# Kernel optimization log

Hardware: AMD Instinct MI355X
Metric: run time of the kernel (lower is better)

The kernel has to match this reference:

```python
import jax, jax.numpy as jnp
import numpy as np

IMG = 640.0  # pixel coordinate range for keypoints


def setup_inputs() -> dict:
    key = jax.random.key(0)
    ks = jax.random.split(key, 16)
    B, N, M, C, D, G = 4, 4096, 4096, 256, 256, 32
    s = 1.0 / np.sqrt(C)
    inp = {
        "nodes_t": jax.random.normal(ks[0], (B, N, C), jnp.float32),
        "nodes_t1": jax.random.normal(ks[1], (B, M, C), jnp.float32),
        "kpts_t1_pred": jax.random.uniform(ks[2], (B, N, 2), jnp.float32) * IMG,
        "kpts_t1_actual": jax.random.uniform(ks[3], (B, M, 2), jnp.float32) * IMG,
        "Wq": jax.random.normal(ks[4], (D, C), jnp.float32) * s,
        "bq": jnp.zeros((D,), jnp.float32),
        "Wk": jax.random.normal(ks[5], (D, C), jnp.float32) * s,
        "bk": jnp.zeros((D,), jnp.float32),
        "Wv": jax.random.normal(ks[6], (D, C), jnp.float32) * s,
        "bv": jnp.zeros((D,), jnp.float32),
        "Wm": jax.random.normal(ks[7], (D, D), jnp.float32) * (1.0 / np.sqrt(D)),
        "bm": jnp.zeros((D,), jnp.float32),
        "Wg1": jax.random.normal(ks[8], (G, 3), jnp.float32) * (1.0 / np.sqrt(3.0)),
        "bg1": jnp.zeros((G,), jnp.float32),
        "Wg2": jax.random.normal(ks[9], (G, G), jnp.float32) * (1.0 / np.sqrt(G)),
        "bg2": jnp.zeros((G,), jnp.float32),
        "iter_idx": 0,
    }
    return inp


def reference(nodes_t, nodes_t1, kpts_t1_pred, kpts_t1_actual,
              Wq, bq, Wk, bk, Wv, bv, Wm, bm, Wg1, bg1, Wg2, bg2, iter_idx):
    # window size schedule (iter_idx is a static Python int)
    win = 64.0 if iter_idx == 0 else max(4.0, 32.0 / 2 ** (iter_idx - 1))

    Q = nodes_t @ Wq.T + bq      # [B,N,256]
    K = nodes_t1 @ Wk.T + bk     # [B,M,256]
    V = nodes_t1 @ Wv.T + bv     # [B,M,256]

    # distance-based window mask [B,N,M]
    du = jnp.abs(kpts_t1_pred[:, :, 0:1] - kpts_t1_actual[:, None, :, 0])
    dv = jnp.abs(kpts_t1_pred[:, :, 1:2] - kpts_t1_actual[:, None, :, 1])
    mask = (du < win) & (dv < win)

    attn = jnp.einsum('bnd,bmd->bnm', Q, K) / jnp.sqrt(jnp.float32(256.0))
    attn = jnp.where(mask, attn, jnp.float32(-1e9))
    w = jax.nn.softmax(attn, axis=-1)

    matched_features = jnp.einsum('bnm,bmd->bnd', w, V)        # [B,N,256]
    matched_kpts = jnp.einsum('bnm,bmc->bnc', w, kpts_t1_actual)  # [B,N,2]

    confidence = jnp.any(mask, axis=-1, keepdims=True).astype(jnp.float32)  # [B,N,1]
    flow_residual = (matched_kpts - kpts_t1_pred) * confidence

    geo_in = jnp.concatenate([flow_residual, confidence], axis=-1)  # [B,N,3]
    h = jax.nn.silu(geo_in @ Wg1.T + bg1)
    geo_temp = h @ Wg2.T + bg2                                   # [B,N,32]

    merged = matched_features @ Wm.T + bm                        # [B,N,256]
    return merged, geo_temp, flow_residual, confidence
```

## Files before the change

### kernel.cpp

```cpp
#include <hip/hip_runtime.h>
#include <hip/hip_bf16.h>

typedef unsigned short ushort;
typedef unsigned int uint;
typedef __bf16 bf16x8 __attribute__((ext_vector_type(8)));
typedef float f32x4 __attribute__((ext_vector_type(4)));
typedef ushort ushort8 __attribute__((ext_vector_type(8)));

#define LOG2E 1.4426950408889634f
#define MFMA16(a,b,c) __builtin_amdgcn_mfma_f32_16x16x32_bf16((a),(b),(c),0,0,0)
#define GLL16(src, dst) __builtin_amdgcn_global_load_lds( \
    (const __attribute__((address_space(1))) void*)(src), \
    (__attribute__((address_space(3))) void*)(dst), 16, 0, 0)
#define GLL4(src, dst) __builtin_amdgcn_global_load_lds( \
    (const __attribute__((address_space(1))) void*)(src), \
    (__attribute__((address_space(3))) void*)(dst), 4, 0, 0)

static __device__ __forceinline__ uint packbf(float lo, float hi) {
  union { __bf16 h[2]; uint u; } x;
  x.h[0] = (__bf16)lo; x.h[1] = (__bf16)hi;
  return x.u;
}
static __device__ __forceinline__ int cellof(float x) {
  int c = (int)(x * 0.015625f);
  return c < 0 ? 0 : (c > 9 ? 9 : c);
}

__global__ __launch_bounds__(256) void cast_weights(
    const float* __restrict__ W0, const float* __restrict__ W1,
    const float* __restrict__ W2, const float* __restrict__ W3,
    __bf16* __restrict__ out,
    int* __restrict__ hist, int* __restrict__ curs, float* __restrict__ meanN)
{
  if (blockIdx.x == 0 && blockIdx.y == 0) {
    int t = threadIdx.x;
    for (int i = t; i < 1024; i += 256) { hist[i] = 0; curs[i] = 0; meanN[i] = 0.f; }
  }
  const int which = blockIdx.y;
  const float* src = which == 0 ? W0 : which == 1 ? W1 : which == 2 ? W2 : W3;
  const int i = (blockIdx.x * 256 + threadIdx.x) * 4;
  f32x4 v = *(const f32x4*)(src + i);
  union { __bf16 h[4]; uint u[2]; } x;
  #pragma unroll
  for (int j = 0; j < 4; j++) x.h[j] = (__bf16)v[j];
  *(uint*)(out + (size_t)which * 65536 + i) = x.u[0];
  *(uint*)(out + (size_t)which * 65536 + i + 2) = x.u[1];
}

__global__ __launch_bounds__(256) void cast_nodes(
    const float* __restrict__ n0, const float* __restrict__ n1,
    __bf16* __restrict__ o0, __bf16* __restrict__ o1)
{
  const float* s = blockIdx.y ? n1 : n0;
  __bf16* o = blockIdx.y ? o1 : o0;
  const int i = (blockIdx.x * 256 + threadIdx.x) * 4;
  f32x4 v = *(const f32x4*)(s + i);
  union { __bf16 h[4]; uint u[2]; } x;
  #pragma unroll
  for (int j = 0; j < 4; j++) x.h[j] = (__bf16)v[j];
  *(uint*)(o + i) = x.u[0];
  *(uint*)(o + i + 2) = x.u[1];
}

__global__ __launch_bounds__(256) void hist_kernel(
    const float* __restrict__ kpred, const float* __restrict__ kact,
    int* __restrict__ hist, int* __restrict__ cellpt)
{
  int p = blockIdx.x * 256 + threadIdx.x;
  int type = p >> 14, idx = p & 16383;
  const float2 c = ((const float2*)(type == 0 ? kpred : kact))[idx];
  int cell = cellof(c.x) * 10 + cellof(c.y);
  int b = idx >> 12;
  atomicAdd(&hist[(type * 4 + b) * 128 + cell], 1);
  cellpt[type * 16384 + idx] = cell;
}

__global__ __launch_bounds__(256) void scan_kernel(
    const int* __restrict__ hist, int* __restrict__ strt, int* __restrict__ curs)
{
  __shared__ int sh[1024];
  int t = threadIdx.x;
  for (int i = t; i < 1024; i += 256) sh[i] = hist[i];
  __syncthreads();
  if (t < 8) {
    int run = 0;
    for (int c = 0; c < 100; c++) {
      strt[t * 128 + c] = run;
      curs[t * 128 + c] = run;
      run += sh[t * 128 + c];
    }
    strt[t * 128 + 100] = run;
  }
}

__global__ __launch_bounds__(256) void scatter_kernel(
    const float* __restrict__ kpred, const float* __restrict__ kact,
    const int* __restrict__ cellpt, int* __restrict__ curs,
    int* __restrict__ sq, int* __restrict__ invq, float* __restrict__ kpS,
    int* __restrict__ sk, int* __restrict__ invk, float* __restrict__ kaS)
{
  int p = blockIdx.x * 256 + threadIdx.x;
  int type = p >> 14, idx = p & 16383;
  int b = idx >> 12, n = idx & 4095;
  int cell = cellpt[type * 16384 + idx];
  int pos = atomicAdd(&curs[(type * 4 + b) * 128 + cell], 1);
  if (type == 0) {
    sq[b * 4096 + pos] = n;
    invq[b * 4096 + n] = pos;
    ((float2*)kpS)[b * 4096 + pos] = ((const float2*)kpred)[idx];
  } else {
    sk[b * 4096 + pos] = n;
    invk[b * 4096 + n] = pos;
    ((float2*)kaS)[b * 4096 + pos] = ((const float2*)kact)[idx];
  }
}

__global__ __launch_bounds__(256) void meansum_kernel(
    const float* __restrict__ nodes_t1, float* __restrict__ meanN)
{
  int b = blockIdx.y, chunk = blockIdx.x, c = threadIdx.x;
  const float* base = nodes_t1 + ((size_t)b * 4096 + chunk * 256) * 256 + c;
  float s = 0.f;
  for (int r = 0; r < 256; r++) s += base[(size_t)r * 256];
  atomicAdd(&meanN[b * 256 + c], s);
}

__global__ __launch_bounds__(256) void vmean_kernel(
    const float* __restrict__ meanN, const float* __restrict__ Wv,
    const float* __restrict__ bv, float* __restrict__ Vmean)
{
  __shared__ float mn[256];
  int b = blockIdx.x, d = threadIdx.x;
  mn[d] = meanN[b * 256 + d] * (1.0f / 4096.0f);
  __syncthreads();
  float s = bv[d];
  const float* w = Wv + (size_t)d * 256;
  for (int c = 0; c < 256; c++) s += mn[c] * w[c];
  Vmean[b * 256 + d] = s;
}

__global__ __launch_bounds__(256) void gemm_qkv(
    const ushort* __restrict__ A0, const ushort* __restrict__ A1,
    const ushort* __restrict__ W4,
    const float* __restrict__ bq, const float* __restrict__ bk,
    const float* __restrict__ bv,
    __bf16* __restrict__ outQ, __bf16* __restrict__ outK,
    __bf16* __restrict__ outVs,
    const int* __restrict__ invq, const int* __restrict__ invk)
{
  const int z = blockIdx.z;
  const ushort* A = z == 0 ? A0 : A1;
  const ushort* Wa = z == 0 ? W4 : W4 + 65536;
  const ushort* Wb = W4 + 131072;
  const int* inv = z == 0 ? invq : invk;

  const int wid = threadIdx.x >> 6;
  const int lane = threadIdx.x & 63;
  const int q = lane & 15, g = lane >> 4;
  const int nb = blockIdx.x * 64 + (wid >> 1) * 32;
  const int db = blockIdx.y * 128 + (wid & 1) * 64;

  f32x4 acc[2][4], accv[2][4];
  #pragma unroll
  for (int a = 0; a < 2; a++)
    #pragma unroll
    for (int b = 0; b < 4; b++) {
      acc[a][b] = f32x4{0.f,0.f,0.f,0.f};
      accv[a][b] = f32x4{0.f,0.f,0.f,0.f};
    }

  const ushort* Wa0 = Wa + (size_t)(db + q) * 256 + g * 8;
  const ushort* Wb0 = Wb + (size_t)(db + q) * 256 + g * 8;
  const ushort* Ar0 = A + (size_t)(nb + q) * 256 + g * 8;
  const ushort* Ar1 = A + (size_t)(nb + 16 + q) * 256 + g * 8;

  #pragma unroll
  for (int c0 = 0; c0 < 256; c0 += 32) {
    bf16x8 a0 = *(const bf16x8*)(Ar0 + c0);
    bf16x8 a1 = *(const bf16x8*)(Ar1 + c0);
    #pragma unroll
    for (int df = 0; df < 4; df++) {
      bf16x8 w = *(const bf16x8*)(Wa0 + df * 16 * 256 + c0);
      acc[0][df] = MFMA16(a0, w, acc[0][df]);
      acc[1][df] = MFMA16(a1, w, acc[1][df]);
    }
    if (z == 1) {
      #pragma unroll
      for (int df = 0; df < 4; df++) {
        bf16x8 w = *(const bf16x8*)(Wb0 + df * 16 * 256 + c0);
        accv[0][df] = MFMA16(a0, w, accv[0][df]);
        accv[1][df] = MFMA16(a1, w, accv[1][df]);
      }
    }
  }
  const float* biasA = z == 0 ? bq : bk;
  __bf16* oA = z == 0 ? outQ : outK;
  #pragma unroll
  for (int df = 0; df < 4; df++) {
    float ba = biasA[db + df * 16 + q];
    float bb = bv[db + df * 16 + q];
    #pragma unroll
    for (int nf = 0; nf < 2; nf++)
      #pragma unroll
      for (int r = 0; r < 4; r++) {
        int row = nb + nf * 16 + g * 4 + r;
        int d = db + df * 16 + q;
        int pos = inv[row];
        size_t orow = (size_t)(row & ~4095) + pos;
        oA[orow * 256 + d] = (__bf16)(acc[nf][df][r] + ba);
        if (z == 1)
          outVs[orow * 256 + d] = (__bf16)(accv[nf][df][r] + bb);
      }
  }
}

__global__ __launch_bounds__(256) void transpose_v(
    const ushort* __restrict__ Vs, ushort* __restrict__ VT)
{
  __shared__ ushort tile[64][76];
  const int b = blockIdx.z, rt = blockIdx.x, dt = blockIdx.y;
  const int tid = threadIdx.x;
  const ushort* src = Vs + ((size_t)b * 4096 + rt * 64) * 256 + dt * 64;
  #pragma unroll
  for (int i = 0; i < 2; i++) {
    int c = tid + i * 256;
    int r = c >> 3, dc = (c & 7) * 8;
    ushort8 v = *(const ushort8*)(src + (size_t)r * 256 + dc);
    #pragma unroll
    for (int j = 0; j < 8; j++) tile[r][dc + j] = v[j];
  }
  __syncthreads();
  ushort* dst = VT + ((size_t)b * 256 + dt * 64) * 4096 + rt * 64;
  #pragma unroll
  for (int i = 0; i < 2; i++) {
    int c = tid + i * 256;
    int d = c >> 3, rc = (c & 7) * 8;
    ushort8 v;
    #pragma unroll
    for (int j = 0; j < 8; j++) v[j] = tile[rc + j][d];
    *(ushort8*)(dst + (size_t)d * 4096 + rc) = v;
  }
}

__global__ __launch_bounds__(256) void gemm_merged(
    const ushort* __restrict__ A, const ushort* __restrict__ W,
    const float* __restrict__ bias, float* __restrict__ out)
{
  const int wid = threadIdx.x >> 6;
  const int lane = threadIdx.x & 63;
  const int q = lane & 15, g = lane >> 4;
  const int nb = blockIdx.x * 64 + (wid >> 1) * 32;
  const int db = blockIdx.y * 128 + (wid & 1) * 64;

  f32x4 acc[2][4];
  #pragma unroll
  for (int a = 0; a < 2; a++)
    #pragma unroll
    for (int b = 0; b < 4; b++) acc[a][b] = f32x4{0.f,0.f,0.f,0.f};

  const ushort* W0 = W + (size_t)(db + q) * 256 + g * 8;
  const ushort* Ar0 = A + (size_t)(nb + q) * 256 + g * 8;
  const ushort* Ar1 = A + (size_t)(nb + 16 + q) * 256 + g * 8;

  #pragma unroll
  for (int c0 = 0; c0 < 256; c0 += 32) {
    bf16x8 a0 = *(const bf16x8*)(Ar0 + c0);
    bf16x8 a1 = *(const bf16x8*)(Ar1 + c0);
    #pragma unroll
    for (int df = 0; df < 4; df++) {
      bf16x8 w = *(const bf16x8*)(W0 + df * 16 * 256 + c0);
      acc[0][df] = MFMA16(a0, w, acc[0][df]);
      acc[1][df] = MFMA16(a1, w, acc[1][df]);
    }
  }
  #pragma unroll
  for (int df = 0; df < 4; df++) {
    float bval = bias[db + df * 16 + q];
    #pragma unroll
    for (int nf = 0; nf < 2; nf++)
      #pragma unroll
      for (int r = 0; r < 4; r++) {
        int row = nb + nf * 16 + g * 4 + r;
        out[(size_t)row * 256 + db + df * 16 + q] = acc[nf][df][r] + bval;
      }
  }
}

__global__ __launch_bounds__(256, 2) void attn_kernel(
    const ushort* __restrict__ Q,
    const ushort* __restrict__ K,
    const ushort* __restrict__ VT,
    const float* __restrict__ kpS,
    const int* __restrict__ iter_idx,
    const int* __restrict__ sq,
    const int* __restrict__ strt,
    const float* __restrict__ kaS,
    const float* __restrict__ Vmean,
    __bf16* __restrict__ matched,
    float* __restrict__ out_flow, float* __restrict__ out_conf)
{
  __shared__ __align__(16) ushort Kl[2][8192];
  __shared__ __align__(16) ushort Vl[2][8192];
  __shared__ __align__(16) float2 Cl[2][32];
  __shared__ int tl_t[132], tl_ks[132], tl_ke[132];
  __shared__ int ntile_s;

  const int tid = threadIdx.x;
  const int wid = tid >> 6, lane = tid & 63;
  const int q = lane & 15, g = lane >> 4;
  const int orig = blockIdx.x;
  const int wgid = (orig & 7) * 50 + (orig >> 3);
  const int batch = wgid / 100;
  const int cell = wgid % 100;

  const int qstart = strt[batch * 128 + cell];
  const int nq = strt[batch * 128 + cell + 1] - qstart;
  if (nq == 0) return;

  const int cu = cell / 10, cv = cell % 10;
  const int c0 = cv > 0 ? cv - 1 : 0, c1 = cv < 9 ? cv + 1 : 9;
  const int* kst = strt + (4 + batch) * 128;

  if (tid == 0) {
    int n = 0;
    int lo = cu > 0 ? cu - 1 : 0, hi = cu < 9 ? cu + 1 : 9;
    for (int cc = lo; cc <= hi; cc++) {
      int ks = kst[cc * 10 + c0];
      int ke = kst[cc * 10 + c1 + 1];
      for (int t = ks & ~31; t < ke; t += 32) {
        tl_t[n] = t; tl_ks[n] = ks; tl_ke[n] = ke; n++;
      }
    }
    ntile_s = n;
  }
  __syncthreads();
  const int ntile = ntile_s;

  const int idx = *iter_idx;
  const float win = (idx == 0) ? 64.0f : fmaxf(4.0f, ldexpf(32.0f, 1 - idx));

  const ushort* Kbase = K + (size_t)batch * 4096 * 256;
  const ushort* VTb = VT + (size_t)batch * 1048576;
  const float* kasf = kaS + (size_t)batch * 8192;
  const float* Vm = Vmean + batch * 256;

  const int npass = (nq + 63) >> 6;

  auto STAGE = [&](int ti, int b) {
    const int t = tl_t[ti];
    #pragma unroll
    for (int j = 0; j < 4; j++) {
      int n = wid * 256 + j * 64 + lane;
      int r = n & 31, u = n >> 5;
      GLL16(Kbase + (size_t)(t + r) * 256 + u * 8,
            &Kl[b][(size_t)(wid * 256 + j * 64) * 8]);
    }
    #pragma unroll
    for (int j = 0; j < 4; j++) {
      int n = wid * 256 + j * 64 + lane;
      int pl = n >> 8, d = n & 255;
      GLL16(VTb + (size_t)d * 4096 + t + pl * 8,
            &Vl[b][(size_t)(wid * 256 + j * 64) * 8]);
    }
    if (wid == 0) GLL4(kasf + t * 2 + lane, &Cl[b][0]);
  };

  int cnt = 0, qi = 0;
  bool active = false;
  float pu = 0.f, pv = 0.f;
  bf16x8 qf[8];
  f32x4 O[16];
  float m_run = -1e9f, l_run = 0.f, u_run = 0.f, v_run = 0.f;

  auto PASS_INIT = [&](int pp) {
    int tbase = pp * 64 + wid * 16;
    active = tbase < nq;
    cnt = active ? min(16, nq - tbase) : 0;
    if (active) {
      int qq = q < cnt ? q : cnt - 1;
      int qsrow = batch * 4096 + qstart + tbase + qq;
      qi = sq[qsrow];
      const ushort* qptr = Q + (size_t)qsrow * 256 + g * 8;
      #pragma unroll
      for (int mf = 0; mf < 8; mf++) qf[mf] = *(const bf16x8*)(qptr + mf * 32);
      float2 kpv = ((const float2*)kpS)[qsrow];
      pu = kpv.x; pv = kpv.y;
    }
    #pragma unroll
    for (int i = 0; i < 16; i++) O[i] = f32x4{0.f,0.f,0.f,0.f};
    m_run = -1e9f; l_run = 0.f; u_run = 0.f; v_run = 0.f;
  };

  auto EPILOGUE = [&]() {
    if (!active) return;
    l_run += __shfl_xor(l_run, 16); l_run += __shfl_xor(l_run, 32);
    u_run += __shfl_xor(u_run, 16); u_run += __shfl_xor(u_run, 32);
    v_run += __shfl_xor(v_run, 16); v_run += __shfl_xor(v_run, 32);
    bool degen = (m_run <= -5e8f) || (l_run == 0.f);
    float rinv = degen ? 0.f : 1.0f / l_run;
    if (g == 0 && q < cnt) {
      float conf = degen ? 0.f : 1.0f;
      int row = batch * 4096 + qi;
      float fu = (u_run * rinv - pu) * conf, fv = (v_run * rinv - pv) * conf;
      ((float2*)out_flow)[row] = float2{fu, fv};
      out_conf[row] = conf;
    }
    #pragma unroll
    for (int r = 0; r < 4; r++) {
      int src = 4 * g + r;
      int qi_r = __shfl(qi, src);
      float il_r = __shfl(rinv, src);
      bool dg_r = (il_r == 0.f);
      if (src < cnt) {
        __bf16* mrow = matched + ((size_t)batch * 4096 + qi_r) * 256;
        #pragma unroll
        for (int df = 0; df < 16; df++) {
          float val = dg_r ? Vm[df * 16 + q] : O[df][r] * il_r;
          mrow[df * 16 + q] = (__bf16)val;
        }
      }
    }
  };

  if (ntile == 0) {
    for (int pp = 0; pp < npass; pp++) { PASS_INIT(pp); EPILOGUE(); }
    return;
  }

  const int total = npass * ntile;
  STAGE(0, 0);
  PASS_INIT(0);

  int i = 0, pp = 0;
  for (int it = 0; it < total; ++it) {
    __syncthreads();
    if (it + 1 < total) {
      int ni = (i + 1 == ntile) ? 0 : i + 1;
      STAGE(ni, (it + 1) & 1);
    }
    const int b = it & 1;

    if (active) {
      const int t = tl_t[i], ks = tl_ks[i], ke = tl_ke[i];

      f32x4 s0a = {0.f,0.f,0.f,0.f}, s0b = {0.f,0.f,0.f,0.f};
      f32x4 s1a = {0.f,0.f,0.f,0.f}, s1b = {0.f,0.f,0.f,0.f};
      #pragma unroll
      for (int mf = 0; mf < 8; mf += 2) {
        bf16x8 ka0 = *(const bf16x8*)&Kl[b][(size_t)(((mf    ) * 4 + g) * 32 + q     ) * 8];
        bf16x8 kb0 = *(const bf16x8*)&Kl[b][(size_t)(((mf + 1) * 4 + g) * 32 + q     ) * 8];
        bf16x8 ka1 = *(const bf16x8*)&Kl[b][(size_t)(((mf    ) * 4 + g) * 32 + q + 16) * 8];
        bf16x8 kb1 = *(const bf16x8*)&Kl[b][(size_t)(((mf + 1) * 4 + g) * 32 + q + 16) * 8];
        s0a = MFMA16(ka0, qf[mf],     s0a);
        s0b = MFMA16(kb0, qf[mf + 1], s0b);
        s1a = MFMA16(ka1, qf[mf],     s1a);
        s1b = MFMA16(kb1, qf[mf + 1], s1b);
      }

      float aus[8], avs[8], sv[8];
      #pragma unroll
      for (int r = 0; r < 4; r++) {
        int jr = t + 4 * g + r;
        float2 cc0 = Cl[b][4 * g + r];
        aus[r] = cc0.x; avs[r] = cc0.y;
        bool val = (jr >= ks && jr < ke);
        float du = fabsf(pu - cc0.x), dv = fabsf(pv - cc0.y);
        float sr = s0a[r] + s0b[r];
        sv[r] = (val && fmaxf(du, dv) < win) ? sr * 0.0625f : -1e9f;

        int jr1 = jr + 16;
        float2 cc1 = Cl[b][16 + 4 * g + r];
        aus[4 + r] = cc1.x; avs[4 + r] = cc1.y;
        val = (jr1 >= ks && jr1 < ke);
        du = fabsf(pu - cc1.x); dv = fabsf(pv - cc1.y);
        sr = s1a[r] + s1b[r];
        sv[4 + r] = (val && fmaxf(du, dv) < win) ? sr * 0.0625f : -1e9f;
      }

      float mt = fmaxf(fmaxf(fmaxf(sv[0], sv[1]), fmaxf(sv[2], sv[3])),
                       fmaxf(fmaxf(sv[4], sv[5]), fmaxf(sv[6], sv[7])));
      mt = fmaxf(mt, __shfl_xor(mt, 16));
      mt = fmaxf(mt, __shfl_xor(mt, 32));
      if (__any(mt > m_run + 8.0f)) {
        float m_new = fmaxf(m_run, mt);
        float scale = exp2f((m_run - m_new) * LOG2E);
        l_run *= scale; u_run *= scale; v_run *= scale;
        float s_r[4];
        #pragma unroll
        for (int r = 0; r < 4; r++) s_r[r] = __shfl(scale, 4 * g + r);
        #pragma unroll
        for (int df = 0; df < 16; df++)
          #pragma unroll
          for (int r = 0; r < 4; r++) O[df][r] *= s_r[r];
        m_run = m_new;
      }

      float p[8];
      #pragma unroll
      for (int ii = 0; ii < 8; ii++) p[ii] = exp2f((sv[ii] - m_run) * LOG2E);
      #pragma unroll
      for (int ii = 0; ii < 8; ii++) {
        l_run += p[ii];
        u_run += p[ii] * aus[ii];
        v_run += p[ii] * avs[ii];
      }

      uint d0 = packbf(p[0], p[1]), d1 = packbf(p[2], p[3]);
      uint d2 = packbf(p[4], p[5]), d3 = packbf(p[6], p[7]);
      int srcA = q + ((g & 1) << 5);
      int srcB = srcA + 16;
      uint x0 = (uint)__shfl((int)d0, srcA), x1 = (uint)__shfl((int)d1, srcA);
      uint x2 = (uint)__shfl((int)d0, srcB), x3 = (uint)__shfl((int)d1, srcB);
      uint y0 = (uint)__shfl((int)d2, srcA), y1 = (uint)__shfl((int)d3, srcA);
      uint y2 = (uint)__shfl((int)d2, srcB), y3 = (uint)__shfl((int)d3, srcB);
      union { uint i4[4]; bf16x8 v; } af;
      bool lo = (g < 2);
      af.i4[0] = lo ? x0 : y0; af.i4[1] = lo ? x1 : y1;
      af.i4[2] = lo ? x2 : y2; af.i4[3] = lo ? x3 : y3;

      #pragma unroll
      for (int df = 0; df < 16; df++) {
        bf16x8 vfd = *(const bf16x8*)&Vl[b][(size_t)(g * 256 + df * 16 + q) * 8];
        O[df] = MFMA16(af.v, vfd, O[df]);
      }
    }

    if (i == ntile - 1) {
      EPILOGUE();
      pp++;
      if (pp < npass) PASS_INIT(pp);
      i = 0;
    } else {
      i++;
    }
  }
}

__global__ __launch_bounds__(256) void geo_kernel(
    const float* __restrict__ flow, const float* __restrict__ conf_in,
    const float* __restrict__ Wg1, const float* __restrict__ bg1,
    const float* __restrict__ Wg2, const float* __restrict__ bg2,
    float* __restrict__ out_geo)
{
  __shared__ float w1[32][3], b1[32], b2[32];
  __shared__ __align__(16) float w2[32][32];
  int tid = threadIdx.x;
  for (int i = tid; i < 96; i += 256) w1[i / 3][i % 3] = Wg1[i];
  if (tid < 32) { b1[tid] = bg1[tid]; b2[tid] = bg2[tid]; }
  for (int i = tid; i < 1024; i += 256) w2[i / 32][i % 32] = Wg2[i];
  __syncthreads();

  int row = blockIdx.x * 256 + tid;
  float2 f = ((const float2*)flow)[row];
  float c = conf_in[row];
  float h[32];
  #pragma unroll
  for (int j = 0; j < 32; j++) {
    float x = w1[j][0] * f.x + w1[j][1] * f.y + w1[j][2] * c + b1[j];
    h[j] = x / (1.f + __expf(-x));
  }
  #pragma unroll
  for (int o = 0; o < 32; o += 2) {
    float s0 = b2[o], s1 = b2[o + 1];
    #pragma unroll
    for (int j = 0; j < 32; j += 4) {
      f32x4 wa = *(const f32x4*)&w2[o][j];
      f32x4 wb = *(const f32x4*)&w2[o + 1][j];
      s0 += wa[0]*h[j] + wa[1]*h[j+1] + wa[2]*h[j+2] + wa[3]*h[j+3];
      s1 += wb[0]*h[j] + wb[1]*h[j+1] + wb[2]*h[j+2] + wb[3]*h[j+3];
    }
    ((float2*)out_geo)[((size_t)row * 32 + o) >> 1] = float2{s0, s1};
  }
}

extern "C" void kernel_launch(void* const* d_in, const int* in_sizes, int n_in,
                              void* d_out, int out_size, void* d_ws, size_t ws_size,
                              hipStream_t stream) {
  const float* nodes_t  = (const float*)d_in[0];
  const float* nodes_t1 = (const float*)d_in[1];
  const float* kpred    = (const float*)d_in[2];
  const float* kact     = (const float*)d_in[3];
  const float* Wq = (const float*)d_in[4];  const float* bq = (const float*)d_in[5];
  const float* Wk = (const float*)d_in[6];  const float* bk = (const float*)d_in[7];
  const float* Wv = (const float*)d_in[8];  const float* bv = (const float*)d_in[9];
  const float* Wm = (const float*)d_in[10]; const float* bm = (const float*)d_in[11];
  const float* Wg1= (const float*)d_in[12]; const float* bg1= (const float*)d_in[13];
  const float* Wg2= (const float*)d_in[14]; const float* bg2= (const float*)d_in[15];
  const int* iter = (const int*)d_in[16];

  float* out_merged = (float*)d_out;
  float* out_geo  = out_merged + 4 * 4096 * 32 * 8;
  out_geo = out_merged + 4 * 4096 * 256;
  float* out_flow = out_geo + 4 * 4096 * 32;
  float* out_conf = out_flow + 4 * 4096 * 2;

  ushort* wsQ   = (ushort*)d_ws;
  ushort* wsK   = wsQ + 4194304;
  ushort* wsVT  = wsK + 4194304;
  ushort* wsM   = wsVT + 4194304;
  ushort* wsW   = wsM + 4194304;
  float*  kaS   = (float*)(wsW + 262144);
  float*  kpS   = kaS + 32768;
  float*  meanN = kpS + 32768;
  float*  Vmean = meanN + 1024;
  int*    hist  = (int*)(Vmean + 1024);
  int*    strt  = hist + 1024;
  int*    curs  = strt + 1024;
  int*    cellpt= curs + 1024;
  int*    sq    = cellpt + 32768;
  int*    sk    = sq + 16384;
  int*    invk  = sk + 16384;
  int*    invq  = invk + 16384;
  ushort* wsA0  = (ushort*)(invq + 16384);
  ushort* wsA1  = wsA0 + 4194304;

  dim3 cg(64, 4, 1);
  cast_weights<<<cg, 256, 0, stream>>>(Wq, Wk, Wv, Wm, (__bf16*)wsW,
                                       hist, curs, meanN);
  dim3 ng(4096, 2, 1);
  cast_nodes<<<ng, 256, 0, stream>>>(nodes_t, nodes_t1,
                                     (__bf16*)wsA0, (__bf16*)wsA1);
  hist_kernel<<<128, 256, 0, stream>>>(kpred, kact, hist, cellpt);
  scan_kernel<<<1, 256, 0, stream>>>(hist, strt, curs);
  scatter_kernel<<<128, 256, 0, stream>>>(kpred, kact, cellpt, curs,
                                          sq, invq, kpS, sk, invk, kaS);
  dim3 mg(16, 4, 1);
  meansum_kernel<<<mg, 256, 0, stream>>>(nodes_t1, meanN);
  vmean_kernel<<<4, 256, 0, stream>>>(meanN, Wv, bv, Vmean);

  dim3 qg(256, 2, 2);
  gemm_qkv<<<qg, 256, 0, stream>>>(wsA0, wsA1, wsW, bq, bk, bv,
                                   (__bf16*)wsQ, (__bf16*)wsK, (__bf16*)wsM,
                                   invq, invk);
  dim3 tg(64, 4, 4);
  transpose_v<<<tg, 256, 0, stream>>>(wsM, wsVT);
  attn_kernel<<<400, 256, 0, stream>>>(wsQ, wsK, wsVT, kpS, iter,
                                       sq, strt, kaS, Vmean,
                                       (__bf16*)wsM, out_flow, out_conf);
  dim3 gg(256, 2, 1);
  gemm_merged<<<gg, 256, 0, stream>>>(wsM, wsW + 196608, bm, out_merged);
  geo_kernel<<<64, 256, 0, stream>>>(out_flow, out_conf, Wg1, bg1, Wg2, bg2, out_geo);
}
```

Baseline: 205.8 us.

## Fuse prep kernels, merge gemm with geo, and XOR-swizzle K/V LDS tiles

Several small setup kernels (weight cast, node cast, histogram, mean-sum) are merged into one launch, with a memset replacing the in-kernel zeroing. Scan and V-mean are merged, and the output GEMM is merged with the geo MLP into one launch. Separately, the attention kernel's K and V shared-memory tiles get an XOR swizzle to reduce LDS bank conflicts on fragment reads. The aim is less launch overhead and fewer conflicts, in exchange for heavier branching inside the fused kernels.

```diff
diff --git a/kernel.cpp b/kernel.cpp
--- a/kernel.cpp
+++ b/kernel.cpp
@@ -26,70 +26,87 @@
   return c < 0 ? 0 : (c > 9 ? 9 : c);
 }
 
-__global__ __launch_bounds__(256) void cast_weights(
-    const float* __restrict__ W0, const float* __restrict__ W1,
-    const float* __restrict__ W2, const float* __restrict__ W3,
-    __bf16* __restrict__ out,
-    int* __restrict__ hist, int* __restrict__ curs, float* __restrict__ meanN)
+__global__ __launch_bounds__(256) void prep_kernel(
+    const float* __restrict__ Wq, const float* __restrict__ Wk,
+    const float* __restrict__ Wv, const float* __restrict__ Wm,
+    __bf16* __restrict__ wsW,
+    const float* __restrict__ n0, const float* __restrict__ n1,
+    __bf16* __restrict__ a0, __bf16* __restrict__ a1,
+    const float* __restrict__ kpred, const float* __restrict__ kact,
+    int* __restrict__ hist, int* __restrict__ cellpt,
+    float* __restrict__ meanN)
 {
-  if (blockIdx.x == 0 && blockIdx.y == 0) {
-    int t = threadIdx.x;
-    for (int i = t; i < 1024; i += 256) { hist[i] = 0; curs[i] = 0; meanN[i] = 0.f; }
-  }
-  const int which = blockIdx.y;
-  const float* src = which == 0 ? W0 : which == 1 ? W1 : which == 2 ? W2 : W3;
-  const int i = (blockIdx.x * 256 + threadIdx.x) * 4;
-  f32x4 v = *(const f32x4*)(src + i);
-  union { __bf16 h[4]; uint u[2]; } x;
-  #pragma unroll
-  for (int j = 0; j < 4; j++) x.h[j] = (__bf16)v[j];
-  *(uint*)(out + (size_t)which * 65536 + i) = x.u[0];
-  *(uint*)(out + (size_t)which * 65536 + i + 2) = x.u[1];
-}
-
-__global__ __launch_bounds__(256) void cast_nodes(
-    const float* __restrict__ n0, const float* __restrict__ n1,
-    __bf16* __restrict__ o0, __bf16* __restrict__ o1)
-{
-  const float* s = blockIdx.y ? n1 : n0;
-  __bf16* o = blockIdx.y ? o1 : o0;
-  const int i = (blockIdx.x * 256 + threadIdx.x) * 4;
-  f32x4 v = *(const f32x4*)(s + i);
-  union { __bf16 h[4]; uint u[2]; } x;
-  #pragma unroll
-  for (int j = 0; j < 4; j++) x.h[j] = (__bf16)v[j];
-  *(uint*)(o + i) = x.u[0];
-  *(uint*)(o + i + 2) = x.u[1];
-}
-
-__global__ __launch_bounds__(256) void hist_kernel(
-    const float* __restrict__ kpred, const float* __restrict__ kact,
-    int* __restrict__ hist, int* __restrict__ cellpt)
-{
-  int p = blockIdx.x * 256 + threadIdx.x;
-  int type = p >> 14, idx = p & 16383;
-  const float2 c = ((const float2*)(type == 0 ? kpred : kact))[idx];
-  int cell = cellof(c.x) * 10 + cellof(c.y);
-  int b = idx >> 12;
-  atomicAdd(&hist[(type * 4 + b) * 128 + cell], 1);
-  cellpt[type * 16384 + idx] = cell;
-}
-
-__global__ __launch_bounds__(256) void scan_kernel(
-    const int* __restrict__ hist, int* __restrict__ strt, int* __restrict__ curs)
+  const int bid = blockIdx.x, tid = threadIdx.x;
+  if (bid < 64) {
+    const int which = bid >> 4;
+    const float* src = which == 0 ? Wq : which == 1 ? Wk : which == 2 ? Wv : Wm;
+    const int i = (bid & 15) * 4096 + tid * 16;
+    #pragma unroll
+    for (int j2 = 0; j2 < 4; j2++) {
+      f32x4 v = *(const f32x4*)(src + i + j2 * 4);
+      union { __bf16 h[4]; uint u[2]; } x;
+      #pragma unroll
+      for (int j = 0; j < 4; j++) x.h[j] = (__bf16)v[j];
+      *(uint*)(wsW + (size_t)which * 65536 + i + j2 * 4) = x.u[0];
+      *(uint*)(wsW + (size_t)which * 65536 + i + j2 * 4 + 2) = x.u[1];
+    }
+  } else if (bid < 8256) {
+    const int k = bid - 64;
+    const float* s = k < 4096 ? n0 : n1;
+    __bf16* o = k < 4096 ? a0 : a1;
+    const int i = (k & 4095) * 1024 + tid * 4;
+    f32x4 v = *(const f32x4*)(s + i);
+    union { __bf16 h[4]; uint u[2]; } x;
+    #pragma unroll
+    for (int j = 0; j < 4; j++) x.h[j] = (__bf16)v[j];
+    *(uint*)(o + i) = x.u[0];
+    *(uint*)(o + i + 2) = x.u[1];
+  } else if (bid < 8384) {
+    const int p = (bid - 8256) * 256 + tid;
+    const int type = p >> 14, idx = p & 16383;
+    const float2 c = ((const float2*)(type == 0 ? kpred : kact))[idx];
+    const int cell = cellof(c.x) * 10 + cellof(c.y);
+    const int b = idx >> 12;
+    atomicAdd(&hist[(type * 4 + b) * 128 + cell], 1);
+    cellpt[type * 16384 + idx] = cell;
+  } else {
+    const int mb = bid - 8384;
+    const int b = mb >> 4, chunk = mb & 15;
+    const float* base = n1 + ((size_t)b * 4096 + chunk * 256) * 256 + tid;
+    float s = 0.f;
+    for (int r = 0; r < 256; r++) s += base[(size_t)r * 256];
+    atomicAdd(&meanN[b * 256 + tid], s);
+  }
+}
+
+__global__ __launch_bounds__(256) void scan_vmean(
+    const int* __restrict__ hist, int* __restrict__ strt, int* __restrict__ curs,
+    const float* __restrict__ meanN, const float* __restrict__ Wv,
+    const float* __restrict__ bv, float* __restrict__ Vmean)
 {
   __shared__ int sh[1024];
-  int t = threadIdx.x;
-  for (int i = t; i < 1024; i += 256) sh[i] = hist[i];
-  __syncthreads();
-  if (t < 8) {
-    int run = 0;
-    for (int c = 0; c < 100; c++) {
-      strt[t * 128 + c] = run;
-      curs[t * 128 + c] = run;
-      run += sh[t * 128 + c];
-    }
-    strt[t * 128 + 100] = run;
+  __shared__ float mn[256];
+  const int t = threadIdx.x;
+  if (blockIdx.x == 0) {
+    for (int i = t; i < 1024; i += 256) sh[i] = hist[i];
+    __syncthreads();
+    if (t < 8) {
+      int run = 0;
+      for (int c = 0; c < 100; c++) {
+        strt[t * 128 + c] = run;
+        curs[t * 128 + c] = run;
+        run += sh[t * 128 + c];
+      }
+      strt[t * 128 + 100] = run;
+    }
+  } else {
+    const int b = blockIdx.x - 1;
+    mn[t] = meanN[b * 256 + t] * (1.0f / 4096.0f);
+    __syncthreads();
+    float s = bv[t];
+    const float* w = Wv + (size_t)t * 256;
+    for (int c = 0; c < 256; c++) s += mn[c] * w[c];
+    Vmean[b * 256 + t] = s;
   }
 }
 
@@ -115,30 +132,6 @@
   }
 }
 
-__global__ __launch_bounds__(256) void meansum_kernel(
-    const float* __restrict__ nodes_t1, float* __restrict__ meanN)
-{
-  int b = blockIdx.y, chunk = blockIdx.x, c = threadIdx.x;
-  const float* base = nodes_t1 + ((size_t)b * 4096 + chunk * 256) * 256 + c;
-  float s = 0.f;
-  for (int r = 0; r < 256; r++) s += base[(size_t)r * 256];
-  atomicAdd(&meanN[b * 256 + c], s);
-}
-
-__global__ __launch_bounds__(256) void vmean_kernel(
-    const float* __restrict__ meanN, const float* __restrict__ Wv,
-    const float* __restrict__ bv, float* __restrict__ Vmean)
-{
-  __shared__ float mn[256];
-  int b = blockIdx.x, d = threadIdx.x;
-  mn[d] = meanN[b * 256 + d] * (1.0f / 4096.0f);
-  __syncthreads();
-  float s = bv[d];
-  const float* w = Wv + (size_t)d * 256;
-  for (int c = 0; c < 256; c++) s += mn[c] * w[c];
-  Vmean[b * 256 + d] = s;
-}
-
 __global__ __launch_bounds__(256) void gemm_qkv(
     const ushort* __restrict__ A0, const ushort* __restrict__ A1,
     const ushort* __restrict__ W4,
@@ -239,50 +232,6 @@
     #pragma unroll
     for (int j = 0; j < 8; j++) v[j] = tile[rc + j][d];
     *(ushort8*)(dst + (size_t)d * 4096 + rc) = v;
-  }
-}
-
-__global__ __launch_bounds__(256) void gemm_merged(
-    const ushort* __restrict__ A, const ushort* __restrict__ W,
-    const float* __restrict__ bias, float* __restrict__ out)
-{
-  const int wid = threadIdx.x >> 6;
-  const int lane = threadIdx.x & 63;
-  const int q = lane & 15, g = lane >> 4;
-  const int nb = blockIdx.x * 64 + (wid >> 1) * 32;
-  const int db = blockIdx.y * 128 + (wid & 1) * 64;
-
-  f32x4 acc[2][4];
-  #pragma unroll
-  for (int a = 0; a < 2; a++)
-    #pragma unroll
-    for (int b = 0; b < 4; b++) acc[a][b] = f32x4{0.f,0.f,0.f,0.f};
-
-  const ushort* W0 = W + (size_t)(db + q) * 256 + g * 8;
-  const ushort* Ar0 = A + (size_t)(nb + q) * 256 + g * 8;
-  const ushort* Ar1 = A + (size_t)(nb + 16 + q) * 256 + g * 8;
-
-  #pragma unroll
-  for (int c0 = 0; c0 < 256; c0 += 32) {
-    bf16x8 a0 = *(const bf16x8*)(Ar0 + c0);
-    bf16x8 a1 = *(const bf16x8*)(Ar1 + c0);
-    #pragma unroll
-    for (int df = 0; df < 4; df++) {
-      bf16x8 w = *(const bf16x8*)(W0 + df * 16 * 256 + c0);
-      acc[0][df] = MFMA16(a0, w, acc[0][df]);
-      acc[1][df] = MFMA16(a1, w, acc[1][df]);
-    }
-  }
-  #pragma unroll
-  for (int df = 0; df < 4; df++) {
-    float bval = bias[db + df * 16 + q];
-    #pragma unroll
-    for (int nf = 0; nf < 2; nf++)
-      #pragma unroll
-      for (int r = 0; r < 4; r++) {
-        int row = nb + nf * 16 + g * 4 + r;
-        out[(size_t)row * 256 + db + df * 16 + q] = acc[nf][df][r] + bval;
-      }
   }
 }
 
@@ -351,15 +300,15 @@
     #pragma unroll
     for (int j = 0; j < 4; j++) {
       int n = wid * 256 + j * 64 + lane;
-      int r = n & 31, u = n >> 5;
-      GLL16(Kbase + (size_t)(t + r) * 256 + u * 8,
+      int r = n >> 5, u = n & 31;
+      GLL16(Kbase + (size_t)(t + r) * 256 + ((u ^ (r & 7)) * 8),
             &Kl[b][(size_t)(wid * 256 + j * 64) * 8]);
     }
     #pragma unroll
     for (int j = 0; j < 4; j++) {
       int n = wid * 256 + j * 64 + lane;
-      int pl = n >> 8, d = n & 255;
-      GLL16(VTb + (size_t)d * 4096 + t + pl * 8,
+      int d = n >> 2, c = n & 3;
+      GLL16(VTb + (size_t)d * 4096 + t + ((c ^ ((d >> 1) & 3)) * 8),
             &Vl[b][(size_t)(wid * 256 + j * 64) * 8]);
     }
     if (wid == 0) GLL4(kasf + t * 2 + lane, &Cl[b][0]);
@@ -447,10 +396,12 @@
       f32x4 s1a = {0.f,0.f,0.f,0.f}, s1b = {0.f,0.f,0.f,0.f};
       #pragma unroll
       for (int mf = 0; mf < 8; mf += 2) {
-        bf16x8 ka0 = *(const bf16x8*)&Kl[b][(size_t)(((mf    ) * 4 + g) * 32 + q     ) * 8];
-        bf16x8 kb0 = *(const bf16x8*)&Kl[b][(size_t)(((mf + 1) * 4 + g) * 32 + q     ) * 8];
-        bf16x8 ka1 = *(const bf16x8*)&Kl[b][(size_t)(((mf    ) * 4 + g) * 32 + q + 16) * 8];
-        bf16x8 kb1 = *(const bf16x8*)&Kl[b][(size_t)(((mf + 1) * 4 + g) * 32 + q + 16) * 8];
+        const int u0 = (mf * 4 + g) ^ (q & 7);
+        const int u1 = ((mf + 1) * 4 + g) ^ (q & 7);
+        bf16x8 ka0 = *(const bf16x8*)&Kl[b][(size_t)(q * 32 + u0) * 8];
+        bf16x8 kb0 = *(const bf16x8*)&Kl[b][(size_t)(q * 32 + u1) * 8];
+        bf16x8 ka1 = *(const bf16x8*)&Kl[b][(size_t)((q + 16) * 32 + u0) * 8];
+        bf16x8 kb1 = *(const bf16x8*)&Kl[b][(size_t)((q + 16) * 32 + u1) * 8];
         s0a = MFMA16(ka0, qf[mf],     s0a);
         s0b = MFMA16(kb0, qf[mf + 1], s0b);
         s1a = MFMA16(ka1, qf[mf],     s1a);
@@ -518,9 +469,10 @@
       af.i4[0] = lo ? x0 : y0; af.i4[1] = lo ? x1 : y1;
       af.i4[2] = lo ? x2 : y2; af.i4[3] = lo ? x3 : y3;
 
+      const int vs = g ^ ((q >> 1) & 3);
       #pragma unroll
       for (int df = 0; df < 16; df++) {
-        bf16x8 vfd = *(const bf16x8*)&Vl[b][(size_t)(g * 256 + df * 16 + q) * 8];
+        bf16x8 vfd = *(const bf16x8*)&Vl[b][(size_t)((df * 16 + q) * 4 + vs) * 8];
         O[df] = MFMA16(af.v, vfd, O[df]);
       }
     }
@@ -536,7 +488,9 @@
   }
 }
 
-__global__ __launch_bounds__(256) void geo_kernel(
+__global__ __launch_bounds__(256) void merged_geo(
+    const ushort* __restrict__ A, const ushort* __restrict__ W,
+    const float* __restrict__ bias, float* __restrict__ out,
     const float* __restrict__ flow, const float* __restrict__ conf_in,
     const float* __restrict__ Wg1, const float* __restrict__ bg1,
     const float* __restrict__ Wg2, const float* __restrict__ bg2,
@@ -544,32 +498,73 @@
 {
   __shared__ float w1[32][3], b1[32], b2[32];
   __shared__ __align__(16) float w2[32][32];
-  int tid = threadIdx.x;
-  for (int i = tid; i < 96; i += 256) w1[i / 3][i % 3] = Wg1[i];
-  if (tid < 32) { b1[tid] = bg1[tid]; b2[tid] = bg2[tid]; }
-  for (int i = tid; i < 1024; i += 256) w2[i / 32][i % 32] = Wg2[i];
-  __syncthreads();
-
-  int row = blockIdx.x * 256 + tid;
-  float2 f = ((const float2*)flow)[row];
-  float c = conf_in[row];
-  float h[32];
-  #pragma unroll
-  for (int j = 0; j < 32; j++) {
-    float x = w1[j][0] * f.x + w1[j][1] * f.y + w1[j][2] * c + b1[j];
-    h[j] = x / (1.f + __expf(-x));
-  }
-  #pragma unroll
-  for (int o = 0; o < 32; o += 2) {
-    float s0 = b2[o], s1 = b2[o + 1];
-    #pragma unroll
-    for (int j = 0; j < 32; j += 4) {
-      f32x4 wa = *(const f32x4*)&w2[o][j];
-      f32x4 wb = *(const f32x4*)&w2[o + 1][j];
-      s0 += wa[0]*h[j] + wa[1]*h[j+1] + wa[2]*h[j+2] + wa[3]*h[j+3];
-      s1 += wb[0]*h[j] + wb[1]*h[j+1] + wb[2]*h[j+2] + wb[3]*h[j+3];
-    }
-    ((float2*)out_geo)[((size_t)row * 32 + o) >> 1] = float2{s0, s1};
+  if (blockIdx.x < 512) {
+    const int wid = threadIdx.x >> 6;
+    const int lane = threadIdx.x & 63;
+    const int q = lane & 15, g = lane >> 4;
+    const int nb = (blockIdx.x >> 1) * 64 + (wid >> 1) * 32;
+    const int db = (blockIdx.x & 1) * 128 + (wid & 1) * 64;
+
+    f32x4 acc[2][4];
+    #pragma unroll
+    for (int a = 0; a < 2; a++)
+      #pragma unroll
+      for (int b = 0; b < 4; b++) acc[a][b] = f32x4{0.f,0.f,0.f,0.f};
+
+    const ushort* W0 = W + (size_t)(db + q) * 256 + g * 8;
+    const ushort* Ar0 = A + (size_t)(nb + q) * 256 + g * 8;
+    const ushort* Ar1 = A + (size_t)(nb + 16 + q) * 256 + g * 8;
+
+    #pragma unroll
+    for (int c0 = 0; c0 < 256; c0 += 32) {
+      bf16x8 a0 = *(const bf16x8*)(Ar0 + c0);
+      bf16x8 a1 = *(const bf16x8*)(Ar1 + c0);
+      #pragma unroll
+      for (int df = 0; df < 4; df++) {
+        bf16x8 w = *(const bf16x8*)(W0 + df * 16 * 256 + c0);
+        acc[0][df] = MFMA16(a0, w, acc[0][df]);
+        acc[1][df] = MFMA16(a1, w, acc[1][df]);
+      }
+    }
+    #pragma unroll
+    for (int df = 0; df < 4; df++) {
+      float bval = bias[db + df * 16 + q];
+      #pragma unroll
+      for (int nf = 0; nf < 2; nf++)
+        #pragma unroll
+        for (int r = 0; r < 4; r++) {
+          int row = nb + nf * 16 + g * 4 + r;
+          out[(size_t)row * 256 + db + df * 16 + q] = acc[nf][df][r] + bval;
+        }
+    }
+  } else {
+    const int tid = threadIdx.x;
+    for (int i = tid; i < 96; i += 256) w1[i / 3][i % 3] = Wg1[i];
+    if (tid < 32) { b1[tid] = bg1[tid]; b2[tid] = bg2[tid]; }
+    for (int i = tid; i < 1024; i += 256) w2[i / 32][i % 32] = Wg2[i];
+    __syncthreads();
+
+    int row = (blockIdx.x - 512) * 256 + tid;
+    float2 f = ((const float2*)flow)[row];
+    float c = conf_in[row];
+    float h[32];
+    #pragma unroll
+    for (int j = 0; j < 32; j++) {
+      float x = w1[j][0] * f.x + w1[j][1] * f.y + w1[j][2] * c + b1[j];
+      h[j] = x / (1.f + __expf(-x));
+    }
+    #pragma unroll
+    for (int o = 0; o < 32; o += 2) {
+      float s0 = b2[o], s1 = b2[o + 1];
+      #pragma unroll
+      for (int j = 0; j < 32; j += 4) {
+        f32x4 wa = *(const f32x4*)&w2[o][j];
+        f32x4 wb = *(const f32x4*)&w2[o + 1][j];
+        s0 += wa[0]*h[j] + wa[1]*h[j+1] + wa[2]*h[j+2] + wa[3]*h[j+3];
+        s1 += wb[0]*h[j] + wb[1]*h[j+1] + wb[2]*h[j+2] + wb[3]*h[j+3];
+      }
+      ((float2*)out_geo)[((size_t)row * 32 + o) >> 1] = float2{s0, s1};
+    }
   }
 }
 
@@ -589,8 +584,7 @@
   const int* iter = (const int*)d_in[16];
 
   float* out_merged = (float*)d_out;
-  float* out_geo  = out_merged + 4 * 4096 * 32 * 8;
-  out_geo = out_merged + 4 * 4096 * 256;
+  float* out_geo  = out_merged + 4 * 4096 * 256;
   float* out_flow = out_geo + 4 * 4096 * 32;
   float* out_conf = out_flow + 4 * 4096 * 2;
 
@@ -601,10 +595,10 @@
   ushort* wsW   = wsM + 4194304;
   float*  kaS   = (float*)(wsW + 262144);
   float*  kpS   = kaS + 32768;
-  float*  meanN = kpS + 32768;
-  float*  Vmean = meanN + 1024;
+  float*  Vmean = kpS + 32768;
   int*    hist  = (int*)(Vmean + 1024);
-  int*    strt  = hist + 1024;
+  float*  meanN = (float*)(hist + 1024);
+  int*    strt  = (int*)(meanN + 1024);
   int*    curs  = strt + 1024;
   int*    cellpt= curs + 1024;
   int*    sq    = cellpt + 32768;
@@ -614,20 +608,15 @@
   ushort* wsA0  = (ushort*)(invq + 16384);
   ushort* wsA1  = wsA0 + 4194304;
 
-  dim3 cg(64, 4, 1);
-  cast_weights<<<cg, 256, 0, stream>>>(Wq, Wk, Wv, Wm, (__bf16*)wsW,
-                                       hist, curs, meanN);
-  dim3 ng(4096, 2, 1);
-  cast_nodes<<<ng, 256, 0, stream>>>(nodes_t, nodes_t1,
-                                     (__bf16*)wsA0, (__bf16*)wsA1);
-  hist_kernel<<<128, 256, 0, stream>>>(kpred, kact, hist, cellpt);
-  scan_kernel<<<1, 256, 0, stream>>>(hist, strt, curs);
+  hipMemsetAsync(hist, 0, 8192, stream);
+
+  prep_kernel<<<8448, 256, 0, stream>>>(Wq, Wk, Wv, Wm, (__bf16*)wsW,
+                                        nodes_t, nodes_t1,
+                                        (__bf16*)wsA0, (__bf16*)wsA1,
+                                        kpred, kact, hist, cellpt, meanN);
+  scan_vmean<<<5, 256, 0, stream>>>(hist, strt, curs, meanN, Wv, bv, Vmean);
   scatter_kernel<<<128, 256, 0, stream>>>(kpred, kact, cellpt, curs,
                                           sq, invq, kpS, sk, invk, kaS);
-  dim3 mg(16, 4, 1);
-  meansum_kernel<<<mg, 256, 0, stream>>>(nodes_t1, meanN);
-  vmean_kernel<<<4, 256, 0, stream>>>(meanN, Wv, bv, Vmean);
-
   dim3 qg(256, 2, 2);
   gemm_qkv<<<qg, 256, 0, stream>>>(wsA0, wsA1, wsW, bq, bk, bv,
                                    (__bf16*)wsQ, (__bf16*)wsK, (__bf16*)wsM,
@@ -637,7 +626,7 @@
   attn_kernel<<<400, 256, 0, stream>>>(wsQ, wsK, wsVT, kpS, iter,
                                        sq, strt, kaS, Vmean,
                                        (__bf16*)wsM, out_flow, out_conf);
-  dim3 gg(256, 2, 1);
-  gemm_merged<<<gg, 256, 0, stream>>>(wsM, wsW + 196608, bm, out_merged);
-  geo_kernel<<<64, 256, 0, stream>>>(out_flow, out_conf, Wg1, bg1, Wg2, bg2, out_geo);
-}
+  merged_geo<<<576, 256, 0, stream>>>(wsM, wsW + 196608, bm, out_merged,
+                                      out_flow, out_conf,
+                                      Wg1, bg1, Wg2, bg2, out_geo);
+}
```

Result: faster. 180.0 us (median of 2 runs) (-12.5%).
